# Kernel tuning notes

Measured on AMD Instinct MI355X. Metric: run time of the kernel, lower is better.

Reference implementation:

```python
import jax, jax.numpy as jnp
import numpy as np

B, S, D, H = 2, 2048, 1024, 16
DH = D // H
EPS = 1e-5
LAMBDA_INIT = 0.8


def setup_inputs() -> dict:
    key = jax.random.key(0)
    ks = jax.random.split(key, 16)
    w_std = 1.0 / np.sqrt(D)
    lam_std = LAMBDA_INIT / np.sqrt(DH)
    return {
        "x": jax.random.normal(ks[0], (B, S, D), jnp.float32),
        # Linear weights stored [in, out] (y = x @ W + b), equivalent to torch W.T
        "Wq": jax.random.normal(ks[1], (D, D), jnp.float32) * w_std,
        "bq": jax.random.normal(ks[2], (D,), jnp.float32) * 0.02,
        "Wk": jax.random.normal(ks[3], (D, D), jnp.float32) * w_std,
        "bk": jax.random.normal(ks[4], (D,), jnp.float32) * 0.02,
        "Wv": jax.random.normal(ks[5], (D, D), jnp.float32) * w_std,
        "bv": jax.random.normal(ks[6], (D,), jnp.float32) * 0.02,
        "Wo": jax.random.normal(ks[7], (D, D), jnp.float32) * w_std,
        "bo": jax.random.normal(ks[8], (D,), jnp.float32) * 0.02,
        "lq1": jax.random.normal(ks[9], (H, DH), jnp.float32) * lam_std,
        "lk1": jax.random.normal(ks[10], (H, DH), jnp.float32) * lam_std,
        "lq2": jax.random.normal(ks[11], (H, DH), jnp.float32) * lam_std,
        "lk2": jax.random.normal(ks[12], (H, DH), jnp.float32) * lam_std,
        # per-head GroupNorm(1, head_dim) affine params (torch default init)
        "gn_w": jnp.ones((H, DH), jnp.float32),
        "gn_b": jnp.zeros((H, DH), jnp.float32),
    }


def reference(x, Wq, bq, Wk, bk, Wv, bv, Wo, bo, lq1, lk1, lq2, lk2, gn_w, gn_b):
    b, s, d = x.shape
    h, dh = lq1.shape
    scale = dh ** -0.5

    q = (x @ Wq + bq).reshape(b, s, h, dh)
    k = (x @ Wk + bk).reshape(b, s, h, dh)
    v = (x @ Wv + bv).reshape(b, s, h, dh)

    # differential lambda per head: exp(<lq1,lk1>) - exp(<lq2,lk2>) + lambda_init
    lam = jnp.exp((lq1 * lk1).sum(-1)) - jnp.exp((lq2 * lk2).sum(-1)) + LAMBDA_INIT  # [H]

    scores = jnp.einsum("bihd,bjhd->bhij", q, k) * scale * lam[None, :, None, None]
    attn = jax.nn.softmax(scores, axis=-1)  # no mask in default call path
    out = jnp.einsum("bhij,bjhd->bihd", attn, v)  # [B,S,H,DH]

    # per-head GroupNorm(1, head_dim): normalize over (seq, head_dim) per (batch, head)
    mean = out.mean(axis=(1, 3), keepdims=True)
    var = out.var(axis=(1, 3), keepdims=True)
    normed = (out - mean) * jax.lax.rsqrt(var + EPS)
    normed = normed * gn_w[None, None, :, :] + gn_b[None, None, :, :]

    y = normed.reshape(b, s, d) @ Wo + bo
    return y
```

## Files before the change

### kernel.cpp

```cpp
#include <hip/hip_runtime.h>

#define S_LEN 2048
#define D_DIM 1024
#define H_NUM 16
#define DH 64
#define EPS_GN 1e-5f
#define LAMBDA_INIT 0.8f

typedef unsigned short bfu;
typedef __attribute__((ext_vector_type(8))) short bf16x8;
typedef __attribute__((ext_vector_type(4))) float f32x4;

union FragU { uint4 u; bf16x8 f; };

__device__ inline float bf2f(bfu u){
  union { unsigned int i; float f; } c; c.i = ((unsigned int)u) << 16; return c.f;
}
__device__ inline bfu f2bf(float f){
  union { float f; unsigned int u; } c; c.f = f;
  unsigned int r = c.u + 0x7fffu + ((c.u >> 16) & 1u);
  return (bfu)(r >> 16);
}
__device__ inline unsigned cvtpk(float lo, float hi){
  unsigned r;
  asm("v_cvt_pk_bf16_f32 %0, %1, %2" : "=v"(r) : "v"(lo), "v"(hi));
  return r;
}
__device__ inline void gload16(const void* g, void* lds){
  __builtin_amdgcn_global_load_lds(
      (const __attribute__((address_space(1))) void*)g,
      (__attribute__((address_space(3))) void*)lds, 16, 0, 0);
}
__device__ inline float ldx(const void* p, size_t i, int isf32){
  return isf32 ? ((const float*)p)[i] : bf2f(((const bfu*)p)[i]);
}
__device__ inline float wave_sum(float x){
  #pragma unroll
  for (int off = 32; off; off >>= 1) x += __shfl_xor(x, off, 64);
  return x;
}

__global__ void lambda_kernel(const void* __restrict__ lq1, const void* __restrict__ lk1,
                              const void* __restrict__ lq2, const void* __restrict__ lk2,
                              const unsigned int* __restrict__ gnw_bits,
                              int* __restrict__ flag, float* __restrict__ lam,
                              float* __restrict__ sums){
  const int isf32 = (gnw_bits[0] == 0x3F800000u) ? 1 : 0;
  int t = threadIdx.x;
  if (t == 0) flag[0] = isf32;
  sums[t] = 0.f;
  if (t < H_NUM){
    float s1 = 0.f, s2 = 0.f;
    for (int d = 0; d < DH; ++d){
      s1 += ldx(lq1, t*DH+d, isf32) * ldx(lk1, t*DH+d, isf32);
      s2 += ldx(lq2, t*DH+d, isf32) * ldx(lk2, t*DH+d, isf32);
    }
    lam[t] = expf(s1) - expf(s2) + LAMBDA_INIT;
  }
}

__global__ __launch_bounds__(256) void prep_all(
    const void* __restrict__ x,
    const void* __restrict__ w0, const void* __restrict__ w1,
    const void* __restrict__ w2, const void* __restrict__ w3,
    const int* __restrict__ flag, bfu* __restrict__ xb, bfu* __restrict__ wt)
{
  const int isf32 = flag[0];
  if (blockIdx.x < 2048){
    size_t i = ((size_t)blockIdx.x * 256 + threadIdx.x) * 8;
    if (isf32){
      const float* xf = (const float*)x;
      float4 a = *(const float4*)(xf + i);
      float4 b = *(const float4*)(xf + i + 4);
      bfu o[8] = {f2bf(a.x),f2bf(a.y),f2bf(a.z),f2bf(a.w),f2bf(b.x),f2bf(b.y),f2bf(b.z),f2bf(b.w)};
      *(uint4*)(xb + i) = *(const uint4*)o;
    } else {
      *(uint4*)(xb + i) = *(const uint4*)((const bfu*)x + i);
    }
    return;
  }
  const int widx = blockIdx.x - 2048;
  const int wsel = widx >> 8, tile = widx & 255;
  const void* W = (wsel==0)?w0:(wsel==1)?w1:(wsel==2)?w2:w3;
  bfu* dst = wt + (size_t)wsel * D_DIM * D_DIM;
  __shared__ float Ts[64][65];
  const int r0 = (tile >> 4) * 64, c0 = (tile & 15) * 64;
  const int ty = threadIdx.x >> 6, tx = threadIdx.x & 63;
  #pragma unroll
  for (int rr = 0; rr < 16; ++rr){
    int row = ty*16 + rr;
    Ts[row][tx] = ldx(W, (size_t)(r0 + row) * D_DIM + c0 + tx, isf32);
  }
  __syncthreads();
  #pragma unroll
  for (int rr = 0; rr < 2; ++rr){
    const int row = rr*32 + (threadIdx.x >> 3);
    const int txg = (threadIdx.x & 7) * 8;
    bfu outv[8];
    #pragma unroll
    for (int k2 = 0; k2 < 8; ++k2) outv[k2] = f2bf(Ts[txg + k2][row]);
    *(uint4*)(dst + (size_t)(c0 + row) * D_DIM + r0 + txg) = *(const uint4*)outv;
  }
}

__global__ __launch_bounds__(256, 3) void qkv_mfma(
    const bfu* __restrict__ xb, const bfu* __restrict__ wt,
    const void* __restrict__ bq, const void* __restrict__ bk, const void* __restrict__ bv,
    const float* __restrict__ lam, const int* __restrict__ flag,
    bfu* __restrict__ qb, bfu* __restrict__ kb, bfu* __restrict__ vt)
{
  const int isf32 = flag[0];
  const int z = blockIdx.z;
  const bfu* Wt = wt + (size_t)z * D_DIM * D_DIM;
  const void* bias = (z==0)?bq:(z==1)?bk:bv;

  __shared__ __align__(16) ushort As[2][128][32];
  __shared__ __align__(16) ushort Bs[2][128][32];
  const int m0 = blockIdx.x * 128, n0 = blockIdx.y * 128;
  const int t = threadIdx.x, w = t >> 6, lane = t & 63;
  const int quad = lane >> 4, l15 = lane & 15;
  const int mbase = (w >> 1) * 64, nbase = (w & 1) * 64;

  const int srow = w*32 + (lane >> 2);
  const int gchunk = (lane & 3) ^ ((lane >> 3) & 3);
  const size_t aoff = (size_t)(m0 + srow) * D_DIM + gchunk*8;
  const size_t boff = (size_t)(n0 + srow) * D_DIM + gchunk*8;

#define STAGE(buf, k0) {                                                  \
    gload16(xb + aoff + (k0),            &As[buf][w*32][0]);              \
    gload16(xb + aoff + 16*D_DIM + (k0), &As[buf][w*32+16][0]);           \
    gload16(Wt + boff + (k0),            &Bs[buf][w*32][0]);              \
    gload16(Wt + boff + 16*D_DIM + (k0), &Bs[buf][w*32+16][0]);           \
  }

  f32x4 acc[4][4];
  #pragma unroll
  for (int i = 0; i < 4; ++i)
    #pragma unroll
    for (int j = 0; j < 4; ++j){ f32x4 zz = {0.f,0.f,0.f,0.f}; acc[i][j] = zz; }

  const int chq = (quad ^ ((l15 >> 1) & 3)) * 8;

  STAGE(0, 0)
  int buf = 0;
  for (int k0 = 0; k0 < D_DIM; k0 += 32){
    if (k0 + 32 < D_DIM){
      STAGE(buf ^ 1, k0 + 32)
      asm volatile("s_waitcnt vmcnt(4)" ::: "memory");
    } else {
      asm volatile("s_waitcnt vmcnt(0)" ::: "memory");
    }
    __builtin_amdgcn_s_barrier();
    FragU af[4], bf[4];
    #pragma unroll
    for (int mt = 0; mt < 4; ++mt) af[mt].u = *(const uint4*)&As[buf][mbase + mt*16 + l15][chq];
    #pragma unroll
    for (int nt = 0; nt < 4; ++nt) bf[nt].u = *(const uint4*)&Bs[buf][nbase + nt*16 + l15][chq];
    #pragma unroll
    for (int mt = 0; mt < 4; ++mt)
      #pragma unroll
      for (int nt = 0; nt < 4; ++nt)
        acc[mt][nt] = __builtin_amdgcn_mfma_f32_16x16x32_bf16(af[mt].f, bf[nt].f, acc[mt][nt], 0, 0, 0);
    __builtin_amdgcn_s_barrier();
    buf ^= 1;
  }
#undef STAGE

  #pragma unroll
  for (int mt = 0; mt < 4; ++mt){
    const int mrow = m0 + mbase + mt*16 + quad*4;
    #pragma unroll
    for (int nt = 0; nt < 4; ++nt){
      const int n = n0 + nbase + nt*16 + l15;
      const float bn = ldx(bias, n, isf32);
      if (z < 2){
        bfu* out = (z == 0) ? qb : kb;
        const float qs = (z == 0) ? 0.18033688f * lam[n >> 6] : 1.0f;
        #pragma unroll
        for (int r = 0; r < 4; ++r)
          out[(size_t)(mrow + r) * D_DIM + n] = f2bf((acc[mt][nt][r] + bn) * qs);
      } else {
        const int b = mrow >> 11, s = mrow & (S_LEN - 1);
        const int h = n >> 6, d = n & 63;
        ushort4 pk;
        pk.x = f2bf(acc[mt][nt][0] + bn); pk.y = f2bf(acc[mt][nt][1] + bn);
        pk.z = f2bf(acc[mt][nt][2] + bn); pk.w = f2bf(acc[mt][nt][3] + bn);
        *(ushort4*)(vt + (((size_t)(b*H_NUM + h)*DH + d)*S_LEN) + s) = pk;
      }
    }
  }
}

__global__ __launch_bounds__(256) void repack_kv(
    const bfu* __restrict__ kb, const bfu* __restrict__ vt,
    bfu* __restrict__ ksw, bfu* __restrict__ vsw)
{
  __shared__ __align__(16) ushort L[64][72];
  const int b = blockIdx.z, hy = blockIdx.y, j0 = blockIdx.x * 64;
  const int t = threadIdx.x;
  if (hy < 16){
    const int h = hy, bh = b*H_NUM + h;
    {
      const int j = t >> 2, seg = (t & 3) * 16;
      const bfu* src = kb + ((size_t)(b*S_LEN + j0 + j)*H_NUM + h)*DH + seg;
      uint4 a = *(const uint4*)src, c = *(const uint4*)(src + 8);
      *(uint4*)&L[j][seg] = a; *(uint4*)&L[j][seg+8] = c;
    }
    __syncthreads();
    #pragma unroll
    for (int half = 0; half < 2; ++half){
      int c16 = half*256 + t;
      int blk = c16 >> 6;
      int l   = c16 & 63;
      int jt = blk >> 1, c = blk & 1;
      int m = l & 15, q = l >> 4;
      uint4 v = *(const uint4*)&L[jt*16 + m][c*32 + q*8];
      bfu* dst = ksw + (((size_t)bh*128 + (j0>>4) + jt)*2 + c)*512 + (size_t)l*8;
      *(uint4*)dst = v;
    }
  } else {
    const int h = hy - 16, bh = b*H_NUM + h;
    {
      const int d = t >> 2, seg = (t & 3) * 16;
      const bfu* src = vt + ((size_t)bh*DH + d)*S_LEN + j0 + seg;
      uint4 a = *(const uint4*)src, c = *(const uint4*)(src + 8);
      *(uint4*)&L[d][seg] = a; *(uint4*)&L[d][seg+8] = c;
    }
    __syncthreads();
    #pragma unroll
    for (int half = 0; half < 2; ++half){
      int c16 = half*256 + t;
      int blk = c16 >> 6;
      int l   = c16 & 63;
      int dt = blk >> 1, jcl = blk & 1;
      int m = l & 15, q = l >> 4;
      const int jb = jcl*32 + 16*(q>>1) + 4*(q&1);
      uint2 v0 = *(const uint2*)&L[dt*16 + m][jb];
      uint2 v1 = *(const uint2*)&L[dt*16 + m][jb + 8];
      uint4 v; v.x = v0.x; v.y = v0.y; v.z = v1.x; v.w = v1.y;
      bfu* dst = vsw + (((size_t)bh*4 + dt)*64 + (j0>>5) + jcl)*512 + (size_t)l*8;
      *(uint4*)dst = v;
    }
  }
}

__global__ __launch_bounds__(256, 2) void attn_mfma(
    const bfu* __restrict__ qb, const bfu* __restrict__ ksw, const bfu* __restrict__ vsw,
    bfu* __restrict__ o, float* __restrict__ sums)
{
  const int wg = blockIdx.x;
  const int swz = (wg & 7) * 64 + (wg >> 3);
  const int g = swz >> 4;
  const int i0 = (swz & 15) * 128;
  const int h = g & 15, b = g >> 4;
  const int t = threadIdx.x, w = t >> 6, lane = t & 63;
  const int quad = lane >> 4, l15 = lane & 15;
  const int bh = g;

  FragU qf[2][2];
  #pragma unroll
  for (int mt = 0; mt < 2; ++mt){
    const bfu* qrow = qb + ((size_t)(b*S_LEN + i0 + w*32 + mt*16 + l15)*H_NUM + h)*DH;
    qf[mt][0].u = *(const uint4*)(qrow + quad*8);
    qf[mt][1].u = *(const uint4*)(qrow + 32 + quad*8);
  }

  const bfu* kbase = ksw + (size_t)bh*131072 + (size_t)lane*8;
  const bfu* vbase = vsw + (size_t)bh*131072 + (size_t)lane*8;

  f32x4 Oacc[2][4];
  #pragma unroll
  for (int mt = 0; mt < 2; ++mt)
    #pragma unroll
    for (int dt = 0; dt < 4; ++dt){ f32x4 zz = {0.f,0.f,0.f,0.f}; Oacc[mt][dt] = zz; }
  f32x4 Lacc[2];
  { f32x4 zz = {0.f,0.f,0.f,0.f}; Lacc[0] = zz; Lacc[1] = zz; }
  FragU ones;
  ones.u.x = ones.u.y = ones.u.z = ones.u.w = 0x3F803F80u;

  FragU kfA[4][2], vfA[2][4], kfB[4][2], vfB[2][4];

#define LOAD_K(KF, J0)                                                          \
  { _Pragma("unroll")                                                           \
    for (int jt = 0; jt < 4; ++jt){                                             \
      const bfu* kr = kbase + (size_t)(((J0)>>4) + jt)*1024;                    \
      KF[jt][0].u = *(const uint4*)kr;                                          \
      KF[jt][1].u = *(const uint4*)(kr + 512);                                  \
    } }
#define LOAD_V(VF, J0)                                                          \
  { _Pragma("unroll")                                                           \
    for (int jt2 = 0; jt2 < 2; ++jt2)                                           \
      _Pragma("unroll")                                                         \
      for (int dt = 0; dt < 4; ++dt)                                            \
        VF[jt2][dt].u = *(const uint4*)(vbase + (size_t)(dt*64 + ((J0)>>5) + jt2)*512); }

#define PIN() { asm volatile("" ::: "memory"); __builtin_amdgcn_sched_barrier(0); }

#define PROCESS(KF, VF)                                                         \
  {                                                                             \
    f32x4 s[2][4];                                                              \
    __builtin_amdgcn_s_setprio(1);                                              \
    _Pragma("unroll")                                                           \
    for (int jt = 0; jt < 4; ++jt){                                             \
      _Pragma("unroll")                                                         \
      for (int mt = 0; mt < 2; ++mt){                                           \
        f32x4 zz = {0.f,0.f,0.f,0.f};                                           \
        zz = __builtin_amdgcn_mfma_f32_16x16x32_bf16(KF[jt][0].f, qf[mt][0].f, zz, 0, 0, 0); \
        zz = __builtin_amdgcn_mfma_f32_16x16x32_bf16(KF[jt][1].f, qf[mt][1].f, zz, 0, 0, 0); \
        s[mt][jt] = zz;                                                         \
      }                                                                         \
    }                                                                           \
    __builtin_amdgcn_s_setprio(0);                                              \
    _Pragma("unroll")                                                           \
    for (int mt = 0; mt < 2; ++mt){                                             \
      _Pragma("unroll")                                                         \
      for (int jt = 0; jt < 4; ++jt){                                           \
        _Pragma("unroll")                                                       \
        for (int r = 0; r < 4; ++r)                                             \
          s[mt][jt][r] = __builtin_exp2f(s[mt][jt][r]);                         \
      }                                                                         \
      _Pragma("unroll")                                                         \
      for (int jt2 = 0; jt2 < 2; ++jt2){                                        \
        unsigned pa0 = cvtpk(s[mt][2*jt2][0],   s[mt][2*jt2][1]);               \
        unsigned pa1 = cvtpk(s[mt][2*jt2][2],   s[mt][2*jt2][3]);               \
        unsigned pb0 = cvtpk(s[mt][2*jt2+1][0], s[mt][2*jt2+1][1]);             \
        unsigned pb1 = cvtpk(s[mt][2*jt2+1][2], s[mt][2*jt2+1][3]);             \
        auto r0 = __builtin_amdgcn_permlane32_swap(pa0, pb0, false, false);     \
        auto r1 = __builtin_amdgcn_permlane32_swap(pa1, pb1, false, false);     \
        FragU pf;                                                               \
        pf.u.x = r0[0]; pf.u.y = r1[0]; pf.u.z = r0[1]; pf.u.w = r1[1];         \
        __builtin_amdgcn_s_setprio(1);                                          \
        _Pragma("unroll")                                                       \
        for (int dt = 0; dt < 4; ++dt)                                          \
          Oacc[mt][dt] = __builtin_amdgcn_mfma_f32_16x16x32_bf16(VF[jt2][dt].f, pf.f, Oacc[mt][dt], 0, 0, 0); \
        Lacc[mt] = __builtin_amdgcn_mfma_f32_16x16x32_bf16(ones.f, pf.f, Lacc[mt], 0, 0, 0); \
        __builtin_amdgcn_s_setprio(0);                                          \
      }                                                                         \
    }                                                                           \
  }

  LOAD_K(kfA, 0)
  LOAD_V(vfA, 0)
  PIN()
  for (int j0 = 0; j0 < S_LEN; j0 += 128){
    LOAD_K(kfB, j0 + 64)
    LOAD_V(vfB, j0 + 64)
    PIN()
    PROCESS(kfA, vfA)
    if (j0 + 128 < S_LEN){
      LOAD_K(kfA, j0 + 128)
      LOAD_V(vfA, j0 + 128)
      PIN()
    }
    PROCESS(kfB, vfB)
  }
#undef LOAD_K
#undef LOAD_V
#undef PROCESS
#undef PIN

  float s1 = 0.f, s2 = 0.f;
  #pragma unroll
  for (int mt = 0; mt < 2; ++mt){
    const float inv = 1.f / Lacc[mt][0];
    bfu* orow = o + ((size_t)(b*S_LEN + i0 + w*32 + mt*16 + l15)*H_NUM + h)*DH;
    #pragma unroll
    for (int dt = 0; dt < 4; ++dt){
      float v0 = Oacc[mt][dt][0]*inv, v1 = Oacc[mt][dt][1]*inv;
      float v2 = Oacc[mt][dt][2]*inv, v3 = Oacc[mt][dt][3]*inv;
      s1 += (v0+v1) + (v2+v3);
      s2 += (v0*v0+v1*v1) + (v2*v2+v3*v3);
      ushort4 pk;
      pk.x = f2bf(v0); pk.y = f2bf(v1); pk.z = f2bf(v2); pk.w = f2bf(v3);
      *(ushort4*)(orow + dt*16 + quad*4) = pk;
    }
  }
  s1 = wave_sum(s1); s2 = wave_sum(s2);
  __shared__ float r1[4], r2[4];
  if (lane == 0){ r1[w] = s1; r2[w] = s2; }
  __syncthreads();
  if (t == 0){
    atomicAdd(&sums[bh*2+0], r1[0]+r1[1]+r1[2]+r1[3]);
    atomicAdd(&sums[bh*2+1], r2[0]+r2[1]+r2[2]+r2[3]);
  }
}

__global__ __launch_bounds__(256) void gn_fold(
    const bfu* __restrict__ wt,
    const void* __restrict__ bo, const float* __restrict__ sums,
    const void* __restrict__ gnw, const void* __restrict__ gnb,
    const int* __restrict__ flag,
    bfu* __restrict__ wt2, float* __restrict__ beta)
{
  const int isf32 = flag[0];
  const int z = blockIdx.y;
  const int t = threadIdx.x;
  const int n = blockIdx.x*16 + (t >> 4);
  const int seg = t & 15;
  const float invN = 1.f / (float)(S_LEN * DH);
  const float s1 = sums[(z*H_NUM + seg)*2], s2 = sums[(z*H_NUM + seg)*2 + 1];
  const float mu = s1 * invN;
  const float ri = rsqrtf(s2 * invN - mu*mu + EPS_GN);
  const bfu* src = wt + (size_t)n * D_DIM + seg*64;
  bfu* dst = wt2 + (size_t)z * D_DIM * D_DIM + (size_t)n * D_DIM + seg*64;
  float bacc = 0.f;
  #pragma unroll
  for (int i0 = 0; i0 < 64; i0 += 8){
    uint4 wv = *(const uint4*)(src + i0);
    const bfu* wp = (const bfu*)&wv;
    bfu outv[8];
    #pragma unroll
    for (int j = 0; j < 8; ++j){
      const int c = seg*64 + i0 + j;
      const float wq = bf2f(wp[j]);
      const float a = ri * ldx(gnw, c, isf32);
      outv[j] = f2bf(wq * a);
      bacc += (ldx(gnb, c, isf32) - mu * a) * wq;
    }
    *(uint4*)(dst + i0) = *(const uint4*)outv;
  }
  #pragma unroll
  for (int off = 1; off < 16; off <<= 1) bacc += __shfl_xor(bacc, off, 64);
  if (seg == 0) beta[z*D_DIM + n] = bacc + ldx(bo, n, isf32);
}

__global__ __launch_bounds__(256, 2) void oproj_mfma(
    const bfu* __restrict__ ob, const bfu* __restrict__ wt2,
    const float* __restrict__ beta, const int* __restrict__ flag, void* __restrict__ y)
{
  const int isf32 = flag[0];
  __shared__ __align__(16) ushort As[2][64][32];
  __shared__ __align__(16) ushort Bs[2][128][32];
  const int m0 = blockIdx.x * 64, n0 = blockIdx.y * 128;
  const int t = threadIdx.x, w = t >> 6, lane = t & 63;
  const int quad = lane >> 4, l15 = lane & 15;
  const int mbase = (w >> 1) * 32, nbase = (w & 1) * 64;
  const int bB = m0 >> 11;
  const bfu* Wt = wt2 + (size_t)bB * D_DIM * D_DIM;
  const float* bet = beta + bB * D_DIM;

  const int gchunk = (lane & 3) ^ ((lane >> 3) & 3);
  const size_t aoff = (size_t)(m0 + w*16 + (lane >> 2)) * D_DIM + gchunk*8;
  const size_t boff = (size_t)(n0 + w*32 + (lane >> 2)) * D_DIM + gchunk*8;

#define STAGE(buf, k0) {                                              \
    gload16(ob + aoff + (k0),            &As[buf][w*16][0]);          \
    gload16(Wt + boff + (k0),            &Bs[buf][w*32][0]);          \
    gload16(Wt + boff + 16*D_DIM + (k0), &Bs[buf][w*32+16][0]);       \
  }

  f32x4 acc[2][4];
  #pragma unroll
  for (int i = 0; i < 2; ++i)
    #pragma unroll
    for (int j = 0; j < 4; ++j){ f32x4 zz = {0.f,0.f,0.f,0.f}; acc[i][j] = zz; }

  const int chq = (quad ^ ((l15 >> 1) & 3)) * 8;

  STAGE(0, 0)
  int buf = 0;
  for (int k0 = 0; k0 < D_DIM; k0 += 32){
    if (k0 + 32 < D_DIM){
      STAGE(buf ^ 1, k0 + 32)
      asm volatile("s_waitcnt vmcnt(3)" ::: "memory");
    } else {
      asm volatile("s_waitcnt vmcnt(0)" ::: "memory");
    }
    __builtin_amdgcn_s_barrier();
    FragU af[2], bfr[4];
    #pragma unroll
    for (int mt = 0; mt < 2; ++mt) af[mt].u = *(const uint4*)&As[buf][mbase + mt*16 + l15][chq];
    #pragma unroll
    for (int nt = 0; nt < 4; ++nt) bfr[nt].u = *(const uint4*)&Bs[buf][nbase + nt*16 + l15][chq];
    #pragma unroll
    for (int mt = 0; mt < 2; ++mt)
      #pragma unroll
      for (int nt = 0; nt < 4; ++nt)
        acc[mt][nt] = __builtin_amdgcn_mfma_f32_16x16x32_bf16(af[mt].f, bfr[nt].f, acc[mt][nt], 0, 0, 0);
    __builtin_amdgcn_s_barrier();
    buf ^= 1;
  }
#undef STAGE

  #pragma unroll
  for (int mt = 0; mt < 2; ++mt){
    const int mrow = m0 + mbase + mt*16 + quad*4;
    #pragma unroll
    for (int nt = 0; nt < 4; ++nt){
      const int n = n0 + nbase + nt*16 + l15;
      const float bn = bet[n];
      #pragma unroll
      for (int r = 0; r < 4; ++r){
        float val = acc[mt][nt][r] + bn;
        if (isf32) ((float*)y)[(size_t)(mrow + r) * D_DIM + n] = val;
        else       ((bfu*)y)[(size_t)(mrow + r) * D_DIM + n] = f2bf(val);
      }
    }
  }
}

extern "C" void kernel_launch(void* const* d_in, const int* in_sizes, int n_in,
                              void* d_out, int out_size, void* d_ws, size_t ws_size,
                              hipStream_t stream)
{
  const void* x   = d_in[0];
  const void* Wq  = d_in[1];
  const void* bq  = d_in[2];
  const void* Wk  = d_in[3];
  const void* bk  = d_in[4];
  const void* Wv  = d_in[5];
  const void* bv  = d_in[6];
  const void* Wo  = d_in[7];
  const void* bo  = d_in[8];
  const void* lq1 = d_in[9];
  const void* lk1 = d_in[10];
  const void* lq2 = d_in[11];
  const void* lk2 = d_in[12];
  const void* gnw = d_in[13];
  const void* gnb = d_in[14];

  float* ws   = (float*)d_ws;
  int*   flag = (int*)d_ws;
  float* lam  = ws + 16;
  float* sums = ws + 48;

  const size_t MB = 1u << 20;
  char* base = (char*)d_ws + 4096;
  bfu* xb  = (bfu*)(base);
  bfu* wt  = (bfu*)(base + 8*MB);
  bfu* qb  = (bfu*)(base + 16*MB);
  bfu* kb  = (bfu*)(base + 24*MB);
  bfu* vt  = (bfu*)(base + 32*MB);
  bfu* ob  = (bfu*)(base + 40*MB);
  bfu* ksw = xb;
  bfu* vsw = kb + 4*MB/2;
  vsw = (bfu*)(base + 44*MB);
  vsw = (bfu*)(base + 48*MB);
  bfu* wt2 = vt;
  float* beta = (float*)(base + 36*MB);

  lambda_kernel<<<1, 64, 0, stream>>>(lq1, lk1, lq2, lk2, (const unsigned int*)gnw, flag, lam, sums);
  prep_all<<<3072, 256, 0, stream>>>(x, Wq, Wk, Wv, Wo, flag, xb, wt);
  qkv_mfma<<<dim3(32, 8, 3), 256, 0, stream>>>(xb, wt, bq, bk, bv, lam, flag, qb, kb, vt);
  repack_kv<<<dim3(32, 32, 2), 256, 0, stream>>>(kb, vt, ksw, vsw);
  attn_mfma<<<512, 256, 0, stream>>>(qb, ksw, vsw, ob, sums);
  gn_fold<<<dim3(64, 2), 256, 0, stream>>>(wt + (size_t)3*D_DIM*D_DIM, bo, sums, gnw, gnb, flag, wt2, beta);
  oproj_mfma<<<dim3(64, 8), 256, 0, stream>>>(ob, wt2, beta, flag, d_out);
}
```

Measured before the change: 247.9 us.

## Fuse K/V repack into QKV GEMM epilogue and lambda setup into prep kernel

The QKV GEMM epilogue now stages each wave's K and V output tile in shared memory and writes it straight into the swizzled MFMA-friendly layouts used by attention. This removes the separate repack_kv kernel and its full read/write round trip of K and V. The lambda/flag/sums initialisation moves into an extra block of prep_all, removing a tiny launch. The cost is a heavier GEMM epilogue with LDS traffic, strided LDS reads for the V transpose, and a workspace layout reshuffle (wt2 now aliases xb, beta moved to base+5MB). The extra block may run concurrently with qkv inputs, but the flag is now computed per block.

```diff
diff --git a/kernel.cpp b/kernel.cpp
--- a/kernel.cpp
+++ b/kernel.cpp
@@ -40,32 +40,31 @@
   return x;
 }
 
-__global__ void lambda_kernel(const void* __restrict__ lq1, const void* __restrict__ lk1,
-                              const void* __restrict__ lq2, const void* __restrict__ lk2,
-                              const unsigned int* __restrict__ gnw_bits,
-                              int* __restrict__ flag, float* __restrict__ lam,
-                              float* __restrict__ sums){
-  const int isf32 = (gnw_bits[0] == 0x3F800000u) ? 1 : 0;
-  int t = threadIdx.x;
-  if (t == 0) flag[0] = isf32;
-  sums[t] = 0.f;
-  if (t < H_NUM){
-    float s1 = 0.f, s2 = 0.f;
-    for (int d = 0; d < DH; ++d){
-      s1 += ldx(lq1, t*DH+d, isf32) * ldx(lk1, t*DH+d, isf32);
-      s2 += ldx(lq2, t*DH+d, isf32) * ldx(lk2, t*DH+d, isf32);
-    }
-    lam[t] = expf(s1) - expf(s2) + LAMBDA_INIT;
-  }
-}
-
 __global__ __launch_bounds__(256) void prep_all(
     const void* __restrict__ x,
     const void* __restrict__ w0, const void* __restrict__ w1,
     const void* __restrict__ w2, const void* __restrict__ w3,
-    const int* __restrict__ flag, bfu* __restrict__ xb, bfu* __restrict__ wt)
+    const unsigned int* __restrict__ gnw_bits,
+    const void* __restrict__ lq1, const void* __restrict__ lk1,
+    const void* __restrict__ lq2, const void* __restrict__ lk2,
+    int* __restrict__ flag, float* __restrict__ lam, float* __restrict__ sums,
+    bfu* __restrict__ xb, bfu* __restrict__ wt)
 {
-  const int isf32 = flag[0];
+  const int isf32 = (gnw_bits[0] == 0x3F800000u) ? 1 : 0;
+  if (blockIdx.x == 3072){
+    int t = threadIdx.x;
+    if (t == 0) flag[0] = isf32;
+    if (t < 64) sums[t] = 0.f;
+    if (t < H_NUM){
+      float s1 = 0.f, s2 = 0.f;
+      for (int d = 0; d < DH; ++d){
+        s1 += ldx(lq1, t*DH+d, isf32) * ldx(lk1, t*DH+d, isf32);
+        s2 += ldx(lq2, t*DH+d, isf32) * ldx(lk2, t*DH+d, isf32);
+      }
+      lam[t] = expf(s1) - expf(s2) + LAMBDA_INIT;
+    }
+    return;
+  }
   if (blockIdx.x < 2048){
     size_t i = ((size_t)blockIdx.x * 256 + threadIdx.x) * 8;
     if (isf32){
@@ -107,7 +106,7 @@
     const bfu* __restrict__ xb, const bfu* __restrict__ wt,
     const void* __restrict__ bq, const void* __restrict__ bk, const void* __restrict__ bv,
     const float* __restrict__ lam, const int* __restrict__ flag,
-    bfu* __restrict__ qb, bfu* __restrict__ kb, bfu* __restrict__ vt)
+    bfu* __restrict__ qb, bfu* __restrict__ ksw, bfu* __restrict__ vsw)
 {
   const int isf32 = flag[0];
   const int z = blockIdx.z;
@@ -166,80 +165,74 @@
   }
 #undef STAGE
 
-  #pragma unroll
-  for (int mt = 0; mt < 4; ++mt){
-    const int mrow = m0 + mbase + mt*16 + quad*4;
-    #pragma unroll
-    for (int nt = 0; nt < 4; ++nt){
-      const int n = n0 + nbase + nt*16 + l15;
-      const float bn = ldx(bias, n, isf32);
-      if (z < 2){
-        bfu* out = (z == 0) ? qb : kb;
-        const float qs = (z == 0) ? 0.18033688f * lam[n >> 6] : 1.0f;
+  if (z == 0){
+    #pragma unroll
+    for (int mt = 0; mt < 4; ++mt){
+      const int mrow = m0 + mbase + mt*16 + quad*4;
+      #pragma unroll
+      for (int nt = 0; nt < 4; ++nt){
+        const int n = n0 + nbase + nt*16 + l15;
+        const float bn = ldx(bias, n, isf32);
+        const float qs = 0.18033688f * lam[n >> 6];
         #pragma unroll
         for (int r = 0; r < 4; ++r)
-          out[(size_t)(mrow + r) * D_DIM + n] = f2bf((acc[mt][nt][r] + bn) * qs);
-      } else {
-        const int b = mrow >> 11, s = mrow & (S_LEN - 1);
-        const int h = n >> 6, d = n & 63;
-        ushort4 pk;
-        pk.x = f2bf(acc[mt][nt][0] + bn); pk.y = f2bf(acc[mt][nt][1] + bn);
-        pk.z = f2bf(acc[mt][nt][2] + bn); pk.w = f2bf(acc[mt][nt][3] + bn);
-        *(ushort4*)(vt + (((size_t)(b*H_NUM + h)*DH + d)*S_LEN) + s) = pk;
+          qb[(size_t)(mrow + r) * D_DIM + n] = f2bf((acc[mt][nt][r] + bn) * qs);
       }
     }
-  }
-}
-
-__global__ __launch_bounds__(256) void repack_kv(
-    const bfu* __restrict__ kb, const bfu* __restrict__ vt,
-    bfu* __restrict__ ksw, bfu* __restrict__ vsw)
-{
-  __shared__ __align__(16) ushort L[64][72];
-  const int b = blockIdx.z, hy = blockIdx.y, j0 = blockIdx.x * 64;
-  const int t = threadIdx.x;
-  if (hy < 16){
-    const int h = hy, bh = b*H_NUM + h;
-    {
-      const int j = t >> 2, seg = (t & 3) * 16;
-      const bfu* src = kb + ((size_t)(b*S_LEN + j0 + j)*H_NUM + h)*DH + seg;
-      uint4 a = *(const uint4*)src, c = *(const uint4*)(src + 8);
-      *(uint4*)&L[j][seg] = a; *(uint4*)&L[j][seg+8] = c;
-    }
-    __syncthreads();
-    #pragma unroll
-    for (int half = 0; half < 2; ++half){
-      int c16 = half*256 + t;
-      int blk = c16 >> 6;
-      int l   = c16 & 63;
-      int jt = blk >> 1, c = blk & 1;
-      int m = l & 15, q = l >> 4;
-      uint4 v = *(const uint4*)&L[jt*16 + m][c*32 + q*8];
-      bfu* dst = ksw + (((size_t)bh*128 + (j0>>4) + jt)*2 + c)*512 + (size_t)l*8;
-      *(uint4*)dst = v;
+    return;
+  }
+
+  ushort* Xw = (w < 2) ? ((ushort*)As + (size_t)w*4096) : ((ushort*)Bs + (size_t)(w-2)*4096);
+  {
+    #pragma unroll
+    for (int mt = 0; mt < 4; ++mt){
+      #pragma unroll
+      for (int nt = 0; nt < 4; ++nt){
+        const int n = n0 + nbase + nt*16 + l15;
+        const float bn = ldx(bias, n, isf32);
+        const int lc = nt*16 + l15;
+        #pragma unroll
+        for (int r = 0; r < 4; ++r){
+          const int lr = mt*16 + quad*4 + r;
+          Xw[lr*64 + lc] = f2bf(acc[mt][nt][r] + bn);
+        }
+      }
+    }
+  }
+  __syncthreads();
+
+  const int b  = m0 >> 11;
+  const int jg0 = (m0 & (S_LEN-1)) + mbase;
+  const int h  = (n0 + nbase) >> 6;
+  const int bh = b*H_NUM + h;
+  const int m = l15, q = quad;
+
+  if (z == 1){
+    #pragma unroll
+    for (int jt = 0; jt < 4; ++jt){
+      #pragma unroll
+      for (int c = 0; c < 2; ++c){
+        uint4 v = *(const uint4*)&Xw[(jt*16 + m)*64 + c*32 + q*8];
+        bfu* dst = ksw + (((size_t)bh*128 + (jg0>>4) + jt)*2 + c)*512 + (size_t)lane*8;
+        *(uint4*)dst = v;
+      }
     }
   } else {
-    const int h = hy - 16, bh = b*H_NUM + h;
-    {
-      const int d = t >> 2, seg = (t & 3) * 16;
-      const bfu* src = vt + ((size_t)bh*DH + d)*S_LEN + j0 + seg;
-      uint4 a = *(const uint4*)src, c = *(const uint4*)(src + 8);
-      *(uint4*)&L[d][seg] = a; *(uint4*)&L[d][seg+8] = c;
-    }
-    __syncthreads();
-    #pragma unroll
-    for (int half = 0; half < 2; ++half){
-      int c16 = half*256 + t;
-      int blk = c16 >> 6;
-      int l   = c16 & 63;
-      int dt = blk >> 1, jcl = blk & 1;
-      int m = l & 15, q = l >> 4;
-      const int jb = jcl*32 + 16*(q>>1) + 4*(q&1);
-      uint2 v0 = *(const uint2*)&L[dt*16 + m][jb];
-      uint2 v1 = *(const uint2*)&L[dt*16 + m][jb + 8];
-      uint4 v; v.x = v0.x; v.y = v0.y; v.z = v1.x; v.w = v1.y;
-      bfu* dst = vsw + (((size_t)bh*4 + dt)*64 + (j0>>5) + jcl)*512 + (size_t)l*8;
-      *(uint4*)dst = v;
+    const int jb = 16*(q>>1) + 4*(q&1);
+    #pragma unroll
+    for (int dt = 0; dt < 4; ++dt){
+      #pragma unroll
+      for (int jcl = 0; jcl < 2; ++jcl){
+        const int jb2 = jcl*32 + jb;
+        bfu o[8];
+        #pragma unroll
+        for (int i = 0; i < 4; ++i){
+          o[i]   = Xw[(jb2 + i)*64     + dt*16 + m];
+          o[4+i] = Xw[(jb2 + 8 + i)*64 + dt*16 + m];
+        }
+        bfu* dst = vsw + (((size_t)bh*4 + dt)*64 + (jg0>>5) + jcl)*512 + (size_t)lane*8;
+        *(uint4*)dst = *(const uint4*)o;
+      }
     }
   }
 }
@@ -529,20 +522,15 @@
   bfu* xb  = (bfu*)(base);
   bfu* wt  = (bfu*)(base + 8*MB);
   bfu* qb  = (bfu*)(base + 16*MB);
-  bfu* kb  = (bfu*)(base + 24*MB);
-  bfu* vt  = (bfu*)(base + 32*MB);
+  bfu* ksw = (bfu*)(base + 24*MB);
+  bfu* vsw = (bfu*)(base + 32*MB);
   bfu* ob  = (bfu*)(base + 40*MB);
-  bfu* ksw = xb;
-  bfu* vsw = kb + 4*MB/2;
-  vsw = (bfu*)(base + 44*MB);
-  vsw = (bfu*)(base + 48*MB);
-  bfu* wt2 = vt;
-  float* beta = (float*)(base + 36*MB);
-
-  lambda_kernel<<<1, 64, 0, stream>>>(lq1, lk1, lq2, lk2, (const unsigned int*)gnw, flag, lam, sums);
-  prep_all<<<3072, 256, 0, stream>>>(x, Wq, Wk, Wv, Wo, flag, xb, wt);
-  qkv_mfma<<<dim3(32, 8, 3), 256, 0, stream>>>(xb, wt, bq, bk, bv, lam, flag, qb, kb, vt);
-  repack_kv<<<dim3(32, 32, 2), 256, 0, stream>>>(kb, vt, ksw, vsw);
+  bfu* wt2 = xb;
+  float* beta = (float*)(base + 5*MB);
+
+  prep_all<<<3073, 256, 0, stream>>>(x, Wq, Wk, Wv, Wo, (const unsigned int*)gnw,
+                                     lq1, lk1, lq2, lk2, flag, lam, sums, xb, wt);
+  qkv_mfma<<<dim3(32, 8, 3), 256, 0, stream>>>(xb, wt, bq, bk, bv, lam, flag, qb, ksw, vsw);
   attn_mfma<<<512, 256, 0, stream>>>(qb, ksw, vsw, ob, sums);
   gn_fold<<<dim3(64, 2), 256, 0, stream>>>(wt + (size_t)3*D_DIM*D_DIM, bo, sums, gnw, gnb, flag, wt2, beta);
   oproj_mfma<<<dim3(64, 8), 256, 0, stream>>>(ob, wt2, beta, flag, d_out);
```

Result: faster. 237.2 us (-4.3%).
